# Optimization experiments

Measured on AMD Instinct MI355X. Metric: run time of the kernel, lower is better.

## Reference

```python
import jax, jax.numpy as jnp
import numpy as np
import math

N_HEAD = 16

def _rope(x):
    # x: [B, H, T, D], D even; interleaved-pair rotation as in the torch code
    B, H, T, D = x.shape
    theta = 10000.0 ** (-2.0 * jnp.arange(D // 2, dtype=x.dtype) / D)  # [D/2]
    pos = jnp.arange(T, dtype=x.dtype)[:, None]                        # [T,1]
    ang = pos * theta[None, :]                                          # [T, D/2]
    sin, cos = jnp.sin(ang), jnp.cos(ang)
    x1, x2 = x[..., ::2], x[..., 1::2]
    x1r = x1 * cos - x2 * sin
    x2r = x1 * sin + x2 * cos
    # re-interleave
    out = jnp.stack([x1r, x2r], axis=-1).reshape(B, H, T, D)
    return out

def setup_inputs() -> dict:
    key = jax.random.key(0)
    ks = jax.random.split(key, 3)
    B, T, C = 4, 2048, 1024
    x = jax.random.normal(ks[0], (B, T, C), dtype=jnp.float32)
    W_qkv = jax.random.normal(ks[1], (C, 3 * C), dtype=jnp.float32) * (1.0 / math.sqrt(C))
    b_qkv = jnp.zeros((3 * C,), dtype=jnp.float32)
    W_proj = jax.random.normal(ks[2], (C, C), dtype=jnp.float32) * (1.0 / math.sqrt(C))
    b_proj = jnp.zeros((C,), dtype=jnp.float32)
    return {"x": x, "W_qkv": W_qkv, "b_qkv": b_qkv, "W_proj": W_proj, "b_proj": b_proj}

def reference(x, W_qkv, b_qkv, W_proj, b_proj):
    B, T, C = x.shape
    H = N_HEAD
    D = C // H
    qkv = x @ W_qkv + b_qkv                      # [B,T,3C]
    q, k, v = jnp.split(qkv, 3, axis=-1)
    def to_heads(t):
        return t.reshape(B, T, H, D).transpose(0, 2, 1, 3)  # [B,H,T,D]
    q, k, v = to_heads(q), to_heads(k), to_heads(v)
    q = _rope(q)
    k = _rope(k)
    att = jnp.einsum('bhqd,bhkd->bhqk', q, k) * (1.0 / math.sqrt(D))
    mask = jnp.tril(jnp.ones((T, T), dtype=bool))
    att = jnp.where(mask[None, None, :, :], att, -jnp.inf)
    att = jax.nn.softmax(att, axis=-1)
    y = jnp.einsum('bhqk,bhkd->bhqd', att, v)    # [B,H,T,D]
    y = y.transpose(0, 2, 1, 3).reshape(B, T, C)
    return y @ W_proj + b_proj
```

## Files before the change

### kernel.cpp

```cpp
#include <hip/hip_runtime.h>
#include <cstddef>

#define B_DIM 4
#define T_DIM 2048
#define C_DIM 1024
#define H_DIM 16
#define D_DIM 64
#define C3_DIM 3072

typedef __attribute__((ext_vector_type(8))) _Float16 f16x8;
typedef __attribute__((ext_vector_type(4))) _Float16 f16x4;
typedef __attribute__((ext_vector_type(4))) float f32x4;

typedef const __attribute__((address_space(1))) unsigned int* gptr_t;
typedef __attribute__((address_space(3))) unsigned int* lptr_t;

#define QSCALE 0.180336850073f
#define NTHETA 0.41524101186f

__global__ __launch_bounds__(256) void prep(
    const float* __restrict__ x, _Float16* __restrict__ xh,
    const float* __restrict__ Wq, _Float16* __restrict__ Wqt,
    const float* __restrict__ Wp, _Float16* __restrict__ Wpt)
{
    __shared__ float tile[64][65];
    const int z = blockIdx.x, tid = threadIdx.x;

    if (z < 8192) {
        size_t i = (size_t)z * 1024 + tid * 4;
        float4 v = *(const float4*)&x[i];
        f16x4 o = { (_Float16)v.x, (_Float16)v.y, (_Float16)v.z, (_Float16)v.w };
        *(f16x4*)&xh[i] = o;
        return;
    }

    const float* W;
    _Float16* Wt;
    int N, idx;
    if (z < 8960) { W = Wq; Wt = Wqt; N = C3_DIM; idx = z - 8192; }
    else          { W = Wp; Wt = Wpt; N = C_DIM;  idx = z - 8960; }
    const int K = C_DIM;
    const int nblk = N / 64;
    const int n0 = (idx % nblk) * 64, k0 = (idx / nblk) * 64;

    const int tx = tid & 15, ty = tid >> 4;
#pragma unroll
    for (int it = 0; it < 4; ++it) {
        int r = it * 16 + ty;
        *(float4*)&tile[r][tx * 4] =
            *(const float4*)&W[(size_t)(k0 + r) * N + n0 + tx * 4];
    }
    __syncthreads();
    int c = tid >> 2, t0 = (tid & 3) * 16;
    __align__(16) _Float16 tmp[16];
#pragma unroll
    for (int j = 0; j < 16; ++j) tmp[j] = (_Float16)tile[t0 + j][c];
    _Float16* o = Wt + (size_t)(n0 + c) * K + k0 + t0;
    *(f16x8*)o = *(f16x8*)&tmp[0];
    *(f16x8*)(o + 8) = *(f16x8*)&tmp[8];
}

#define STAGE4(BUF, KK)                                                       \
    do {                                                                      \
        __builtin_amdgcn_global_load_lds((gptr_t)(const void*)(ag + (KK)),    \
            (lptr_t)(void*)&Af[BUF][w * 2 + 0][0][0], 16, 0, 0);              \
        __builtin_amdgcn_global_load_lds(                                     \
            (gptr_t)(const void*)(ag + (KK) + 16 * K),                        \
            (lptr_t)(void*)&Af[BUF][w * 2 + 1][0][0], 16, 0, 0);              \
        __builtin_amdgcn_global_load_lds((gptr_t)(const void*)(bg + (KK)),    \
            (lptr_t)(void*)&Bf[BUF][w * 2 + 0][0][0], 16, 0, 0);              \
        __builtin_amdgcn_global_load_lds(                                     \
            (gptr_t)(const void*)(bg + (KK) + 16 * K),                        \
            (lptr_t)(void*)&Bf[BUF][w * 2 + 1][0][0], 16, 0, 0);              \
    } while (0)

#define COMPUTE32(CUR, SWAPPED)                                               \
    do {                                                                      \
        f16x8 av[4], bv[4];                                                   \
        _Pragma("unroll")                                                     \
        for (int i = 0; i < 4; ++i) {                                         \
            av[i] = *(const f16x8*)&Af[CUR][wm * 4 + i][lane][0];             \
            bv[i] = *(const f16x8*)&Bf[CUR][wn * 4 + i][lane][0];             \
        }                                                                     \
        _Pragma("unroll")                                                     \
        for (int i = 0; i < 4; ++i)                                           \
            _Pragma("unroll")                                                 \
            for (int j = 0; j < 4; ++j)                                       \
                acc[i][j] = (SWAPPED)                                         \
                    ? __builtin_amdgcn_mfma_f32_16x16x32_f16(                 \
                          bv[j], av[i], acc[i][j], 0, 0, 0)                   \
                    : __builtin_amdgcn_mfma_f32_16x16x32_f16(                 \
                          av[i], bv[j], acc[i][j], 0, 0, 0);                  \
    } while (0)

#define KLOOP(SWAPPED)                                                        \
    do {                                                                      \
        STAGE4(0, 0);                                                         \
        int cur = 0;                                                          \
        for (int kt = 0; kt < K / 32 - 1; ++kt) {                             \
            STAGE4(cur ^ 1, (kt + 1) * 32);                                   \
            asm volatile("s_waitcnt vmcnt(4)" ::: "memory");                  \
            __builtin_amdgcn_s_barrier();                                     \
            COMPUTE32(cur, SWAPPED);                                          \
            __builtin_amdgcn_s_barrier();                                     \
            cur ^= 1;                                                         \
        }                                                                     \
        asm volatile("s_waitcnt vmcnt(0)" ::: "memory");                      \
        __builtin_amdgcn_s_barrier();                                         \
        COMPUTE32(cur, SWAPPED);                                              \
    } while (0)

__global__ __launch_bounds__(256) void gemm_qkv(
    const _Float16* __restrict__ A, const _Float16* __restrict__ Bt,
    const float* __restrict__ bias,
    _Float16* __restrict__ Qb, _Float16* __restrict__ Kb, _Float16* __restrict__ Vt)
{
    __shared__ __align__(16) _Float16 Af[2][8][64][8];
    __shared__ __align__(16) _Float16 Bf[2][8][64][8];
    const int tid = threadIdx.x;
    const int lane = tid & 63, w = tid >> 6;
    const int lm = lane & 15, lq = lane >> 4;
    const int wm = w >> 1, wn = w & 1;
    const int m0 = blockIdx.y * 128, n0 = blockIdx.x * 128;
    const int K = C_DIM;

    const _Float16* ag = A + (size_t)(m0 + w * 32 + lm) * K + lq * 8;
    const _Float16* bg = Bt + (size_t)(n0 + w * 32 + lm) * K + lq * 8;

    f32x4 acc[4][4];
#pragma unroll
    for (int i = 0; i < 4; ++i)
#pragma unroll
        for (int j = 0; j < 4; ++j) acc[i][j] = (f32x4){0.f, 0.f, 0.f, 0.f};

    const bool is_v = (n0 >= 2 * C_DIM);

    if (!is_v) {
        KLOOP(true);

        const bool is_q = (n0 < C_DIM);
        const float scale = is_q ? QSCALE : 1.0f;
        _Float16* dstbase = is_q ? Qb : Kb;
#pragma unroll
        for (int j = 0; j < 4; ++j) {
            int col = n0 + wn * 64 + j * 16 + lq * 4;
            int d0 = col & 63;
            int h = (col & (C_DIM - 1)) >> 6;
            float4 b4 = *(const float4*)&bias[col];
            float th0 = exp2f(-NTHETA * (float)(d0 >> 1));
            float th1 = exp2f(-NTHETA * (float)((d0 >> 1) + 1));
#pragma unroll
            for (int i = 0; i < 4; ++i) {
                int tg = m0 + wm * 64 + i * 16 + lm;
                int bb = tg >> 11, tl = tg & (T_DIM - 1);
                float v0 = acc[i][j][0] + b4.x;
                float v1 = acc[i][j][1] + b4.y;
                float v2 = acc[i][j][2] + b4.z;
                float v3 = acc[i][j][3] + b4.w;
                float s0, c0, s1, c1;
                __sincosf((float)tl * th0, &s0, &c0);
                __sincosf((float)tl * th1, &s1, &c1);
                f16x4 o = { (_Float16)((v0 * c0 - v1 * s0) * scale),
                            (_Float16)((v0 * s0 + v1 * c0) * scale),
                            (_Float16)((v2 * c1 - v3 * s1) * scale),
                            (_Float16)((v2 * s1 + v3 * c1) * scale) };
                *(f16x4*)&dstbase[((size_t)(bb * 16 + h) * T_DIM + tl) * 64 + d0] = o;
            }
        }
    } else {
        KLOOP(false);

#pragma unroll
        for (int i = 0; i < 4; ++i) {
            int t4 = m0 + wm * 64 + i * 16 + lq * 4;
            int bb = t4 >> 11, tl = t4 & (T_DIM - 1);
#pragma unroll
            for (int j = 0; j < 4; ++j) {
                int col = n0 + wn * 64 + j * 16 + lm;
                int dfull = col - 2 * C_DIM;
                int h = dfull >> 6, d = dfull & 63;
                float bc = bias[col];
                f16x4 o = { (_Float16)(acc[i][j][0] + bc),
                            (_Float16)(acc[i][j][1] + bc),
                            (_Float16)(acc[i][j][2] + bc),
                            (_Float16)(acc[i][j][3] + bc) };
                *(f16x4*)&Vt[((size_t)(bb * 16 + h) * 64 + d) * T_DIM + tl] = o;
            }
        }
    }
}

template <bool OUT_HALF>
__global__ __launch_bounds__(256) void gemm_bt(
    const _Float16* __restrict__ A, const _Float16* __restrict__ Bt,
    const float* __restrict__ bias, void* __restrict__ Cout,
    int M, int N, int K)
{
    __shared__ __align__(16) _Float16 Af[2][8][64][8];
    __shared__ __align__(16) _Float16 Bf[2][8][64][8];
    const int tid = threadIdx.x;
    const int lane = tid & 63, w = tid >> 6;
    const int lm = lane & 15, lq = lane >> 4;
    const int wm = w >> 1, wn = w & 1;
    const int m0 = blockIdx.y * 128, n0 = blockIdx.x * 128;

    const _Float16* ag = A + (size_t)(m0 + w * 32 + lm) * K + lq * 8;
    const _Float16* bg = Bt + (size_t)(n0 + w * 32 + lm) * K + lq * 8;

    f32x4 acc[4][4];
#pragma unroll
    for (int i = 0; i < 4; ++i)
#pragma unroll
        for (int j = 0; j < 4; ++j) acc[i][j] = (f32x4){0.f, 0.f, 0.f, 0.f};

    KLOOP(true);

#pragma unroll
    for (int i = 0; i < 4; ++i) {
        size_t row = (size_t)(m0 + wm * 64 + i * 16 + lm);
#pragma unroll
        for (int j = 0; j < 4; ++j) {
            int col = n0 + wn * 64 + j * 16 + lq * 4;
            float4 b4 = *(const float4*)&bias[col];
            float v0 = acc[i][j][0] + b4.x;
            float v1 = acc[i][j][1] + b4.y;
            float v2 = acc[i][j][2] + b4.z;
            float v3 = acc[i][j][3] + b4.w;
            if (OUT_HALF) {
                f16x4 o = { (_Float16)v0, (_Float16)v1, (_Float16)v2, (_Float16)v3 };
                *(f16x4*)&((_Float16*)Cout)[row * N + col] = o;
            } else {
                float4 o = make_float4(v0, v1, v2, v3);
                *(float4*)&((float*)Cout)[row * N + col] = o;
            }
        }
    }
}

__global__ __launch_bounds__(256) void attn_mfma(
    const _Float16* __restrict__ Qb, const _Float16* __restrict__ Kb,
    const _Float16* __restrict__ Vt, _Float16* __restrict__ yb)
{
    __shared__ __align__(16) _Float16 Kf[8][64][8];
    __shared__ __align__(16) _Float16 Vf[8][64][8];
    __shared__ __align__(16) _Float16 Pb[4][16][72];

    const int tid = threadIdx.x;
    const int bh = blockIdx.x;
    const int qt = 31 - blockIdx.y;
    const int b = bh >> 4, h = bh & 15;
    const int lane = tid & 63, w = tid >> 6;
    const int m = lane & 15, qq = lane >> 4;

    const _Float16* qrow = Qb +
        ((size_t)bh * T_DIM + qt * 64 + w * 16 + m) * D_DIM + qq * 8;
    f16x8 qreg[2];
    qreg[0] = *(const f16x8*)qrow;
    qreg[1] = *(const f16x8*)(qrow + 32);

    float m_i = -1e30f, l_i = 0.f;
    f32x4 acc[4];
#pragma unroll
    for (int db = 0; db < 4; ++db) acc[db] = (f32x4){0.f, 0.f, 0.f, 0.f};

    const _Float16* kg0 = Kb + (size_t)bh * T_DIM * D_DIM +
                          (size_t)(w * 16 + m) * D_DIM + qq * 8;
    const _Float16* vg0 = Vt + (size_t)bh * D_DIM * T_DIM +
                          (size_t)(w * 16 + m) * T_DIM + qq * 8;

    f16x8 kr0 = *(const f16x8*)(kg0);
    f16x8 kr1 = *(const f16x8*)(kg0 + 32);
    f16x8 vr0 = *(const f16x8*)(vg0);
    f16x8 vr1 = *(const f16x8*)(vg0 + 32);

    for (int kt = 0; kt <= qt; ++kt) {
        __syncthreads();
        *(f16x8*)&Kf[w * 2 + 0][lane][0] = kr0;
        *(f16x8*)&Kf[w * 2 + 1][lane][0] = kr1;
        *(f16x8*)&Vf[w * 2 + 0][lane][0] = vr0;
        *(f16x8*)&Vf[w * 2 + 1][lane][0] = vr1;
        __syncthreads();

        int ktn = (kt < qt) ? kt + 1 : kt;
        kr0 = *(const f16x8*)(kg0 + (size_t)ktn * 64 * D_DIM);
        kr1 = *(const f16x8*)(kg0 + (size_t)ktn * 64 * D_DIM + 32);
        vr0 = *(const f16x8*)(vg0 + ktn * 64);
        vr1 = *(const f16x8*)(vg0 + ktn * 64 + 32);

        f32x4 sv[4];
#pragma unroll
        for (int nb = 0; nb < 4; ++nb) {
            f32x4 s = (f32x4){0.f, 0.f, 0.f, 0.f};
            s = __builtin_amdgcn_mfma_f32_16x16x32_f16(
                *(const f16x8*)&Kf[nb * 2 + 0][lane][0], qreg[0], s, 0, 0, 0);
            s = __builtin_amdgcn_mfma_f32_16x16x32_f16(
                *(const f16x8*)&Kf[nb * 2 + 1][lane][0], qreg[1], s, 0, 0, 0);
            sv[nb] = s;
        }

        if (kt == qt) {
            int qlocal = w * 16 + m;
#pragma unroll
            for (int nb = 0; nb < 4; ++nb) {
                int tb = nb * 16 + qq * 4;
#pragma unroll
                for (int r = 0; r < 4; ++r)
                    if (tb + r > qlocal) sv[nb][r] = -1e30f;
            }
        }

        float mt0 = fmaxf(fmaxf(sv[0][0], sv[0][1]), fmaxf(sv[0][2], sv[0][3]));
        float mt1 = fmaxf(fmaxf(sv[1][0], sv[1][1]), fmaxf(sv[1][2], sv[1][3]));
        float mt2 = fmaxf(fmaxf(sv[2][0], sv[2][1]), fmaxf(sv[2][2], sv[2][3]));
        float mt3 = fmaxf(fmaxf(sv[3][0], sv[3][1]), fmaxf(sv[3][2], sv[3][3]));
        float mt = fmaxf(fmaxf(mt0, mt1), fmaxf(mt2, mt3));
        mt = fmaxf(mt, __shfl_xor(mt, 16));
        mt = fmaxf(mt, __shfl_xor(mt, 32));
        float mnew = fmaxf(m_i, mt);
        float alpha = exp2f(m_i - mnew);
        float ll = 0.f;
#pragma unroll
        for (int nb = 0; nb < 4; ++nb) {
            float p0 = exp2f(sv[nb][0] - mnew);
            float p1 = exp2f(sv[nb][1] - mnew);
            float p2 = exp2f(sv[nb][2] - mnew);
            float p3 = exp2f(sv[nb][3] - mnew);
            sv[nb][0] = p0; sv[nb][1] = p1; sv[nb][2] = p2; sv[nb][3] = p3;
            ll += (p0 + p1) + (p2 + p3);
        }
        ll += __shfl_xor(ll, 16);
        ll += __shfl_xor(ll, 32);
        l_i = l_i * alpha + ll;
        m_i = mnew;
#pragma unroll
        for (int db = 0; db < 4; ++db) {
            acc[db][0] *= alpha; acc[db][1] *= alpha;
            acc[db][2] *= alpha; acc[db][3] *= alpha;
        }

#pragma unroll
        for (int nb = 0; nb < 4; ++nb) {
            f16x4 pv = { (_Float16)sv[nb][0], (_Float16)sv[nb][1],
                         (_Float16)sv[nb][2], (_Float16)sv[nb][3] };
            *(f16x4*)&Pb[w][m][nb * 16 + qq * 4] = pv;
        }

        f16x8 pf0 = *(const f16x8*)&Pb[w][m][0 * 32 + qq * 8];
        f16x8 pf1 = *(const f16x8*)&Pb[w][m][1 * 32 + qq * 8];

#pragma unroll
        for (int db = 0; db < 4; ++db) {
            acc[db] = __builtin_amdgcn_mfma_f32_16x16x32_f16(
                *(const f16x8*)&Vf[db * 2 + 0][lane][0], pf0, acc[db], 0, 0, 0);
            acc[db] = __builtin_amdgcn_mfma_f32_16x16x32_f16(
                *(const f16x8*)&Vf[db * 2 + 1][lane][0], pf1, acc[db], 0, 0, 0);
        }
    }

    float inv = 1.0f / l_i;
    _Float16* yrow = yb + (size_t)(b * T_DIM + qt * 64 + w * 16 + m) * C_DIM +
                     h * D_DIM + qq * 4;
#pragma unroll
    for (int db = 0; db < 4; ++db) {
        f16x4 o = { (_Float16)(acc[db][0] * inv), (_Float16)(acc[db][1] * inv),
                    (_Float16)(acc[db][2] * inv), (_Float16)(acc[db][3] * inv) };
        *(f16x4*)(yrow + db * 16) = o;
    }
}

extern "C" void kernel_launch(void* const* d_in, const int* in_sizes, int n_in,
                              void* d_out, int out_size, void* d_ws, size_t ws_size,
                              hipStream_t stream)
{
    const float* x     = (const float*)d_in[0];
    const float* Wqkv  = (const float*)d_in[1];
    const float* bqkv  = (const float*)d_in[2];
    const float* Wproj = (const float*)d_in[3];
    const float* bproj = (const float*)d_in[4];
    float* out = (float*)d_out;

    char* ws = (char*)d_ws;
    _Float16* xh  = (_Float16*)(ws);
    _Float16* yh  = (_Float16*)(ws + 16777216ull);
    _Float16* Qb  = (_Float16*)(ws + 33554432ull);
    _Float16* Kb  = (_Float16*)(ws + 50331648ull);
    _Float16* Vt  = (_Float16*)(ws + 67108864ull);
    _Float16* Wqt = (_Float16*)(ws + 83886080ull);
    _Float16* Wpt = (_Float16*)(ws + 90177536ull);

    dim3 blk(256);

    prep<<<dim3(9216), blk, 0, stream>>>(x, xh, Wqkv, Wqt, Wproj, Wpt);

    gemm_qkv<<<dim3(C3_DIM / 128, (B_DIM * T_DIM) / 128), blk, 0, stream>>>(
        xh, Wqt, bqkv, Qb, Kb, Vt);

    attn_mfma<<<dim3(B_DIM * H_DIM, T_DIM / 64), blk, 0, stream>>>(
        Qb, Kb, Vt, yh);

    gemm_bt<false><<<dim3(C_DIM / 128, (B_DIM * T_DIM) / 128), blk, 0, stream>>>(
        yh, Wpt, bproj, out, B_DIM * T_DIM, C_DIM, C_DIM);
}
```

Measured before the change: 313.8 us.

## Shrink GEMM tiles to 128x64, drop LDS double-buffering, raise occupancy

```diff
diff --git a/kernel.cpp b/kernel.cpp
--- a/kernel.cpp
+++ b/kernel.cpp
@@ -60,76 +60,56 @@
     *(f16x8*)(o + 8) = *(f16x8*)&tmp[8];
 }
 
-#define STAGE4(BUF, KK)                                                       \
+#define KLOOP(SWAPPED)                                                        \
     do {                                                                      \
-        __builtin_amdgcn_global_load_lds((gptr_t)(const void*)(ag + (KK)),    \
-            (lptr_t)(void*)&Af[BUF][w * 2 + 0][0][0], 16, 0, 0);              \
-        __builtin_amdgcn_global_load_lds(                                     \
-            (gptr_t)(const void*)(ag + (KK) + 16 * K),                        \
-            (lptr_t)(void*)&Af[BUF][w * 2 + 1][0][0], 16, 0, 0);              \
-        __builtin_amdgcn_global_load_lds((gptr_t)(const void*)(bg + (KK)),    \
-            (lptr_t)(void*)&Bf[BUF][w * 2 + 0][0][0], 16, 0, 0);              \
-        __builtin_amdgcn_global_load_lds(                                     \
-            (gptr_t)(const void*)(bg + (KK) + 16 * K),                        \
-            (lptr_t)(void*)&Bf[BUF][w * 2 + 1][0][0], 16, 0, 0);              \
-    } while (0)
-
-#define COMPUTE32(CUR, SWAPPED)                                               \
-    do {                                                                      \
-        f16x8 av[4], bv[4];                                                   \
-        _Pragma("unroll")                                                     \
-        for (int i = 0; i < 4; ++i) {                                         \
-            av[i] = *(const f16x8*)&Af[CUR][wm * 4 + i][lane][0];             \
-            bv[i] = *(const f16x8*)&Bf[CUR][wn * 4 + i][lane][0];             \
-        }                                                                     \
-        _Pragma("unroll")                                                     \
-        for (int i = 0; i < 4; ++i)                                           \
+        for (int k0 = 0; k0 < K; k0 += 32) {                                  \
+            __syncthreads();                                                  \
+            __builtin_amdgcn_global_load_lds((gptr_t)(const void*)(ag + k0),  \
+                (lptr_t)(void*)&Af[w * 2 + 0][0][0], 16, 0, 0);               \
+            __builtin_amdgcn_global_load_lds(                                 \
+                (gptr_t)(const void*)(ag + k0 + 16 * K),                      \
+                (lptr_t)(void*)&Af[w * 2 + 1][0][0], 16, 0, 0);               \
+            __builtin_amdgcn_global_load_lds((gptr_t)(const void*)(bg + k0),  \
+                (lptr_t)(void*)&Bf[w][0][0], 16, 0, 0);                       \
+            __syncthreads();                                                  \
+            f16x8 av[2], bv[4];                                               \
+            _Pragma("unroll")                                                 \
+            for (int i = 0; i < 2; ++i)                                       \
+                av[i] = *(const f16x8*)&Af[w * 2 + i][lane][0];               \
             _Pragma("unroll")                                                 \
             for (int j = 0; j < 4; ++j)                                       \
-                acc[i][j] = (SWAPPED)                                         \
-                    ? __builtin_amdgcn_mfma_f32_16x16x32_f16(                 \
-                          bv[j], av[i], acc[i][j], 0, 0, 0)                   \
-                    : __builtin_amdgcn_mfma_f32_16x16x32_f16(                 \
-                          av[i], bv[j], acc[i][j], 0, 0, 0);                  \
+                bv[j] = *(const f16x8*)&Bf[j][lane][0];                       \
+            _Pragma("unroll")                                                 \
+            for (int i = 0; i < 2; ++i)                                       \
+                _Pragma("unroll")                                             \
+                for (int j = 0; j < 4; ++j)                                   \
+                    acc[i][j] = (SWAPPED)                                     \
+                        ? __builtin_amdgcn_mfma_f32_16x16x32_f16(             \
+                              bv[j], av[i], acc[i][j], 0, 0, 0)               \
+                        : __builtin_amdgcn_mfma_f32_16x16x32_f16(             \
+                              av[i], bv[j], acc[i][j], 0, 0, 0);              \
+        }                                                                     \
     } while (0)
 
-#define KLOOP(SWAPPED)                                                        \
-    do {                                                                      \
-        STAGE4(0, 0);                                                         \
-        int cur = 0;                                                          \
-        for (int kt = 0; kt < K / 32 - 1; ++kt) {                             \
-            STAGE4(cur ^ 1, (kt + 1) * 32);                                   \
-            asm volatile("s_waitcnt vmcnt(4)" ::: "memory");                  \
-            __builtin_amdgcn_s_barrier();                                     \
-            COMPUTE32(cur, SWAPPED);                                          \
-            __builtin_amdgcn_s_barrier();                                     \
-            cur ^= 1;                                                         \
-        }                                                                     \
-        asm volatile("s_waitcnt vmcnt(0)" ::: "memory");                      \
-        __builtin_amdgcn_s_barrier();                                         \
-        COMPUTE32(cur, SWAPPED);                                              \
-    } while (0)
-
-__global__ __launch_bounds__(256) void gemm_qkv(
+__global__ __launch_bounds__(256, 4) void gemm_qkv(
     const _Float16* __restrict__ A, const _Float16* __restrict__ Bt,
     const float* __restrict__ bias,
     _Float16* __restrict__ Qb, _Float16* __restrict__ Kb, _Float16* __restrict__ Vt)
 {
-    __shared__ __align__(16) _Float16 Af[2][8][64][8];
-    __shared__ __align__(16) _Float16 Bf[2][8][64][8];
+    __shared__ __align__(16) _Float16 Af[8][64][8];
+    __shared__ __align__(16) _Float16 Bf[4][64][8];
     const int tid = threadIdx.x;
     const int lane = tid & 63, w = tid >> 6;
     const int lm = lane & 15, lq = lane >> 4;
-    const int wm = w >> 1, wn = w & 1;
-    const int m0 = blockIdx.y * 128, n0 = blockIdx.x * 128;
+    const int m0 = blockIdx.y * 128, n0 = blockIdx.x * 64;
     const int K = C_DIM;
 
     const _Float16* ag = A + (size_t)(m0 + w * 32 + lm) * K + lq * 8;
-    const _Float16* bg = Bt + (size_t)(n0 + w * 32 + lm) * K + lq * 8;
-
-    f32x4 acc[4][4];
-#pragma unroll
-    for (int i = 0; i < 4; ++i)
+    const _Float16* bg = Bt + (size_t)(n0 + w * 16 + lm) * K + lq * 8;
+
+    f32x4 acc[2][4];
+#pragma unroll
+    for (int i = 0; i < 2; ++i)
 #pragma unroll
         for (int j = 0; j < 4; ++j) acc[i][j] = (f32x4){0.f, 0.f, 0.f, 0.f};
 
@@ -143,15 +123,15 @@
         _Float16* dstbase = is_q ? Qb : Kb;
 #pragma unroll
         for (int j = 0; j < 4; ++j) {
-            int col = n0 + wn * 64 + j * 16 + lq * 4;
+            int col = n0 + j * 16 + lq * 4;
             int d0 = col & 63;
             int h = (col & (C_DIM - 1)) >> 6;
             float4 b4 = *(const float4*)&bias[col];
             float th0 = exp2f(-NTHETA * (float)(d0 >> 1));
             float th1 = exp2f(-NTHETA * (float)((d0 >> 1) + 1));
 #pragma unroll
-            for (int i = 0; i < 4; ++i) {
-                int tg = m0 + wm * 64 + i * 16 + lm;
+            for (int i = 0; i < 2; ++i) {
+                int tg = m0 + w * 32 + i * 16 + lm;
                 int bb = tg >> 11, tl = tg & (T_DIM - 1);
                 float v0 = acc[i][j][0] + b4.x;
                 float v1 = acc[i][j][1] + b4.y;
@@ -171,12 +151,12 @@
         KLOOP(false);
 
 #pragma unroll
-        for (int i = 0; i < 4; ++i) {
-            int t4 = m0 + wm * 64 + i * 16 + lq * 4;
+        for (int i = 0; i < 2; ++i) {
+            int t4 = m0 + w * 32 + i * 16 + lq * 4;
             int bb = t4 >> 11, tl = t4 & (T_DIM - 1);
 #pragma unroll
             for (int j = 0; j < 4; ++j) {
-                int col = n0 + wn * 64 + j * 16 + lm;
+                int col = n0 + j * 16 + lm;
                 int dfull = col - 2 * C_DIM;
                 int h = dfull >> 6, d = dfull & 63;
                 float bc = bias[col];
@@ -191,36 +171,35 @@
 }
 
 template <bool OUT_HALF>
-__global__ __launch_bounds__(256) void gemm_bt(
+__global__ __launch_bounds__(256, 4) void gemm_bt(
     const _Float16* __restrict__ A, const _Float16* __restrict__ Bt,
     const float* __restrict__ bias, void* __restrict__ Cout,
     int M, int N, int K)
 {
-    __shared__ __align__(16) _Float16 Af[2][8][64][8];
-    __shared__ __align__(16) _Float16 Bf[2][8][64][8];
+    __shared__ __align__(16) _Float16 Af[8][64][8];
+    __shared__ __align__(16) _Float16 Bf[4][64][8];
     const int tid = threadIdx.x;
     const int lane = tid & 63, w = tid >> 6;
     const int lm = lane & 15, lq = lane >> 4;
-    const int wm = w >> 1, wn = w & 1;
-    const int m0 = blockIdx.y * 128, n0 = blockIdx.x * 128;
+    const int m0 = blockIdx.y * 128, n0 = blockIdx.x * 64;
 
     const _Float16* ag = A + (size_t)(m0 + w * 32 + lm) * K + lq * 8;
-    const _Float16* bg = Bt + (size_t)(n0 + w * 32 + lm) * K + lq * 8;
-
-    f32x4 acc[4][4];
-#pragma unroll
-    for (int i = 0; i < 4; ++i)
+    const _Float16* bg = Bt + (size_t)(n0 + w * 16 + lm) * K + lq * 8;
+
+    f32x4 acc[2][4];
+#pragma unroll
+    for (int i = 0; i < 2; ++i)
 #pragma unroll
         for (int j = 0; j < 4; ++j) acc[i][j] = (f32x4){0.f, 0.f, 0.f, 0.f};
 
     KLOOP(true);
 
 #pragma unroll
-    for (int i = 0; i < 4; ++i) {
-        size_t row = (size_t)(m0 + wm * 64 + i * 16 + lm);
+    for (int i = 0; i < 2; ++i) {
+        size_t row = (size_t)(m0 + w * 32 + i * 16 + lm);
 #pragma unroll
         for (int j = 0; j < 4; ++j) {
-            int col = n0 + wn * 64 + j * 16 + lq * 4;
+            int col = n0 + j * 16 + lq * 4;
             float4 b4 = *(const float4*)&bias[col];
             float v0 = acc[i][j][0] + b4.x;
             float v1 = acc[i][j][1] + b4.y;
@@ -392,12 +371,12 @@
 
     prep<<<dim3(9216), blk, 0, stream>>>(x, xh, Wqkv, Wqt, Wproj, Wpt);
 
-    gemm_qkv<<<dim3(C3_DIM / 128, (B_DIM * T_DIM) / 128), blk, 0, stream>>>(
+    gemm_qkv<<<dim3(C3_DIM / 64, (B_DIM * T_DIM) / 128), blk, 0, stream>>>(
         xh, Wqt, bqkv, Qb, Kb, Vt);
 
     attn_mfma<<<dim3(B_DIM * H_DIM, T_DIM / 64), blk, 0, stream>>>(
         Qb, Kb, Vt, yh);
 
-    gemm_bt<false><<<dim3(C_DIM / 128, (B_DIM * T_DIM) / 128), blk, 0, stream>>>(
+    gemm_bt<false><<<dim3(C_DIM / 64, (B_DIM * T_DIM) / 128), blk, 0, stream>>>(
         yh, Wpt, bproj, out, B_DIM * T_DIM, C_DIM, C_DIM);
 }
```

New measurement: 361.3 us. 15.1% more time.

## Enlarge GEMM tiles to 256x128 with 8 waves and split-K-slice pipelining

Applied to the files above, without the earlier changes.

```diff
diff --git a/kernel.cpp b/kernel.cpp
--- a/kernel.cpp
+++ b/kernel.cpp
@@ -60,28 +60,27 @@
     *(f16x8*)(o + 8) = *(f16x8*)&tmp[8];
 }
 
-#define STAGE4(BUF, KK)                                                       \
+#define ISSUE_SLICE(BUF, S, KT)                                               \
     do {                                                                      \
-        __builtin_amdgcn_global_load_lds((gptr_t)(const void*)(ag + (KK)),    \
-            (lptr_t)(void*)&Af[BUF][w * 2 + 0][0][0], 16, 0, 0);              \
-        __builtin_amdgcn_global_load_lds(                                     \
-            (gptr_t)(const void*)(ag + (KK) + 16 * K),                        \
-            (lptr_t)(void*)&Af[BUF][w * 2 + 1][0][0], 16, 0, 0);              \
-        __builtin_amdgcn_global_load_lds((gptr_t)(const void*)(bg + (KK)),    \
-            (lptr_t)(void*)&Bf[BUF][w * 2 + 0][0][0], 16, 0, 0);              \
-        __builtin_amdgcn_global_load_lds(                                     \
-            (gptr_t)(const void*)(bg + (KK) + 16 * K),                        \
-            (lptr_t)(void*)&Bf[BUF][w * 2 + 1][0][0], 16, 0, 0);              \
+        const _Float16* agk = ag + (KT) * 64 + (S) * 32;                      \
+        const _Float16* bgk = bg + (KT) * 64 + (S) * 32;                      \
+        __builtin_amdgcn_global_load_lds((gptr_t)(const void*)(agk),          \
+            (lptr_t)(void*)&Af[BUF][S][w * 2 + 0][0][0], 16, 0, 0);           \
+        __builtin_amdgcn_global_load_lds((gptr_t)(const void*)(agk + 16 * K), \
+            (lptr_t)(void*)&Af[BUF][S][w * 2 + 1][0][0], 16, 0, 0);           \
+        __builtin_amdgcn_global_load_lds((gptr_t)(const void*)(bgk),          \
+            (lptr_t)(void*)&Bf[BUF][S][w][0][0], 16, 0, 0);                   \
     } while (0)
 
-#define COMPUTE32(CUR, SWAPPED)                                               \
+#define COMPUTE_SLICE(BUF, S, SWAPPED)                                        \
     do {                                                                      \
         f16x8 av[4], bv[4];                                                   \
         _Pragma("unroll")                                                     \
         for (int i = 0; i < 4; ++i) {                                         \
-            av[i] = *(const f16x8*)&Af[CUR][wm * 4 + i][lane][0];             \
-            bv[i] = *(const f16x8*)&Bf[CUR][wn * 4 + i][lane][0];             \
+            av[i] = *(const f16x8*)&Af[BUF][S][wm * 4 + i][lane][0];          \
+            bv[i] = *(const f16x8*)&Bf[BUF][S][wn * 4 + i][lane][0];          \
         }                                                                     \
+        __builtin_amdgcn_s_setprio(1);                                        \
         _Pragma("unroll")                                                     \
         for (int i = 0; i < 4; ++i)                                           \
             _Pragma("unroll")                                                 \
@@ -91,41 +90,52 @@
                           bv[j], av[i], acc[i][j], 0, 0, 0)                   \
                     : __builtin_amdgcn_mfma_f32_16x16x32_f16(                 \
                           av[i], bv[j], acc[i][j], 0, 0, 0);                  \
+        __builtin_amdgcn_s_setprio(0);                                        \
     } while (0)
 
 #define KLOOP(SWAPPED)                                                        \
     do {                                                                      \
-        STAGE4(0, 0);                                                         \
-        int cur = 0;                                                          \
-        for (int kt = 0; kt < K / 32 - 1; ++kt) {                             \
-            STAGE4(cur ^ 1, (kt + 1) * 32);                                   \
-            asm volatile("s_waitcnt vmcnt(4)" ::: "memory");                  \
+        const int NT = K / 64;                                                \
+        ISSUE_SLICE(0, 0, 0);                                                 \
+        ISSUE_SLICE(0, 1, 0);                                                 \
+        for (int t = 0; t < NT - 1; ++t) {                                    \
+            const int cb = t & 1, nb = cb ^ 1;                                \
+            ISSUE_SLICE(nb, 0, t + 1);                                        \
+            asm volatile("s_waitcnt vmcnt(6)" ::: "memory");                  \
             __builtin_amdgcn_s_barrier();                                     \
-            COMPUTE32(cur, SWAPPED);                                          \
+            COMPUTE_SLICE(cb, 0, SWAPPED);                                    \
+            ISSUE_SLICE(nb, 1, t + 1);                                        \
+            asm volatile("s_waitcnt vmcnt(6)" ::: "memory");                  \
             __builtin_amdgcn_s_barrier();                                     \
-            cur ^= 1;                                                         \
+            COMPUTE_SLICE(cb, 1, SWAPPED);                                    \
         }                                                                     \
-        asm volatile("s_waitcnt vmcnt(0)" ::: "memory");                      \
-        __builtin_amdgcn_s_barrier();                                         \
-        COMPUTE32(cur, SWAPPED);                                              \
+        {                                                                     \
+            const int cb = (NT - 1) & 1;                                      \
+            asm volatile("s_waitcnt vmcnt(3)" ::: "memory");                  \
+            __builtin_amdgcn_s_barrier();                                     \
+            COMPUTE_SLICE(cb, 0, SWAPPED);                                    \
+            asm volatile("s_waitcnt vmcnt(0)" ::: "memory");                  \
+            __builtin_amdgcn_s_barrier();                                     \
+            COMPUTE_SLICE(cb, 1, SWAPPED);                                    \
+        }                                                                     \
     } while (0)
 
-__global__ __launch_bounds__(256) void gemm_qkv(
+__global__ __launch_bounds__(512, 2) void gemm_qkv(
     const _Float16* __restrict__ A, const _Float16* __restrict__ Bt,
     const float* __restrict__ bias,
     _Float16* __restrict__ Qb, _Float16* __restrict__ Kb, _Float16* __restrict__ Vt)
 {
-    __shared__ __align__(16) _Float16 Af[2][8][64][8];
-    __shared__ __align__(16) _Float16 Bf[2][8][64][8];
+    __shared__ __align__(16) _Float16 Af[2][2][16][64][8];
+    __shared__ __align__(16) _Float16 Bf[2][2][8][64][8];
     const int tid = threadIdx.x;
     const int lane = tid & 63, w = tid >> 6;
     const int lm = lane & 15, lq = lane >> 4;
     const int wm = w >> 1, wn = w & 1;
-    const int m0 = blockIdx.y * 128, n0 = blockIdx.x * 128;
+    const int m0 = blockIdx.y * 256, n0 = blockIdx.x * 128;
     const int K = C_DIM;
 
     const _Float16* ag = A + (size_t)(m0 + w * 32 + lm) * K + lq * 8;
-    const _Float16* bg = Bt + (size_t)(n0 + w * 32 + lm) * K + lq * 8;
+    const _Float16* bg = Bt + (size_t)(n0 + w * 16 + lm) * K + lq * 8;
 
     f32x4 acc[4][4];
 #pragma unroll
@@ -191,21 +201,21 @@
 }
 
 template <bool OUT_HALF>
-__global__ __launch_bounds__(256) void gemm_bt(
+__global__ __launch_bounds__(512, 2) void gemm_bt(
     const _Float16* __restrict__ A, const _Float16* __restrict__ Bt,
     const float* __restrict__ bias, void* __restrict__ Cout,
     int M, int N, int K)
 {
-    __shared__ __align__(16) _Float16 Af[2][8][64][8];
-    __shared__ __align__(16) _Float16 Bf[2][8][64][8];
+    __shared__ __align__(16) _Float16 Af[2][2][16][64][8];
+    __shared__ __align__(16) _Float16 Bf[2][2][8][64][8];
     const int tid = threadIdx.x;
     const int lane = tid & 63, w = tid >> 6;
     const int lm = lane & 15, lq = lane >> 4;
     const int wm = w >> 1, wn = w & 1;
-    const int m0 = blockIdx.y * 128, n0 = blockIdx.x * 128;
+    const int m0 = blockIdx.y * 256, n0 = blockIdx.x * 128;
 
     const _Float16* ag = A + (size_t)(m0 + w * 32 + lm) * K + lq * 8;
-    const _Float16* bg = Bt + (size_t)(n0 + w * 32 + lm) * K + lq * 8;
+    const _Float16* bg = Bt + (size_t)(n0 + w * 16 + lm) * K + lq * 8;
 
     f32x4 acc[4][4];
 #pragma unroll
@@ -388,16 +398,14 @@
     _Float16* Wqt = (_Float16*)(ws + 83886080ull);
     _Float16* Wpt = (_Float16*)(ws + 90177536ull);
 
-    dim3 blk(256);
-
-    prep<<<dim3(9216), blk, 0, stream>>>(x, xh, Wqkv, Wqt, Wproj, Wpt);
-
-    gemm_qkv<<<dim3(C3_DIM / 128, (B_DIM * T_DIM) / 128), blk, 0, stream>>>(
+    prep<<<dim3(9216), dim3(256), 0, stream>>>(x, xh, Wqkv, Wqt, Wproj, Wpt);
+
+    gemm_qkv<<<dim3(C3_DIM / 128, (B_DIM * T_DIM) / 256), dim3(512), 0, stream>>>(
         xh, Wqt, bqkv, Qb, Kb, Vt);
 
-    attn_mfma<<<dim3(B_DIM * H_DIM, T_DIM / 64), blk, 0, stream>>>(
+    attn_mfma<<<dim3(B_DIM * H_DIM, T_DIM / 64), dim3(256), 0, stream>>>(
         Qb, Kb, Vt, yh);
 
-    gemm_bt<false><<<dim3(C_DIM / 128, (B_DIM * T_DIM) / 128), blk, 0, stream>>>(
+    gemm_bt<false><<<dim3(C_DIM / 128, (B_DIM * T_DIM) / 256), dim3(512), 0, stream>>>(
         yh, Wpt, bproj, out, B_DIM * T_DIM, C_DIM, C_DIM);
 }
```

Result: faster. 289.4 us (-7.8%).
